# Performance work log

Hardware: AMD Instinct MI355X
Metric: run time of the kernel (lower is better)

Reference implementation:

```python
import jax, jax.numpy as jnp
import numpy as np

V = 50000
E = 300000
B = 4
LAT = 512
H = 128
L = 3


def setup_inputs() -> dict:
    key = jax.random.key(0)
    ks = jax.random.split(key, 8)
    vertex_xyz = jax.random.normal(ks[0], (V, 3), jnp.float32)
    latent = jax.random.normal(ks[1], (B, LAT), jnp.float32)
    edge_index = jax.random.randint(ks[2], (2, E), 0, V, dtype=jnp.int32)
    def lin(k, out_f, in_f):
        return jax.random.normal(k, (out_f, in_f), jnp.float32) / np.float32(np.sqrt(in_f))
    W_in = lin(ks[3], H, LAT + 3)
    b_in = jnp.zeros((H,), jnp.float32)
    conv_W = jax.random.normal(ks[4], (L, H, H), jnp.float32) / np.float32(np.sqrt(H))
    conv_b = jnp.zeros((L, H), jnp.float32)
    W_out = lin(ks[5], 3, H)
    b_out = jnp.zeros((3,), jnp.float32)
    return dict(vertex_xyz=vertex_xyz, latent=latent, edge_index=edge_index,
                W_in=W_in, b_in=b_in, conv_W=conv_W, conv_b=conv_b,
                W_out=W_out, b_out=b_out)


def _edge_norm(edge_index, B_, V_):
    """GCN symmetric normalization for edge_index tiled B times (same node ids,
    as in the original code's edge_index.repeat(1, B)) plus self-loops on all
    N = B*V flattened nodes. Structure is identical across layers, so compute once."""
    N = B_ * V_
    ei = jnp.tile(edge_index, (1, B_))                 # (2, E*B), ids in [0, V)
    loops = jnp.arange(N, dtype=edge_index.dtype)
    row = jnp.concatenate([ei[0], loops])              # source
    col = jnp.concatenate([ei[1], loops])              # target
    deg = jax.ops.segment_sum(jnp.ones(row.shape, jnp.float32), col, num_segments=N)
    dis = jnp.where(deg > 0, jax.lax.rsqrt(jnp.maximum(deg, 1.0)), 0.0)
    norm = dis[row] * dis[col]                         # (E*B + N,)
    return row, col, norm, N


def reference(vertex_xyz, latent, edge_index, W_in, b_in, conv_W, conv_b, W_out, b_out):
    B_, V_ = latent.shape[0], vertex_xyz.shape[0]
    row, col, norm, N = _edge_norm(edge_index, B_, V_)

    # concat template xyz with broadcast latent -> (B*V, LAT+3)
    x = jnp.concatenate([
        jnp.broadcast_to(vertex_xyz[None], (B_, V_, 3)),
        jnp.broadcast_to(latent[:, None, :], (B_, V_, latent.shape[-1])),
    ], axis=-1).reshape(B_ * V_, -1)

    x = jax.nn.relu(x @ W_in.T + b_in)                 # (N, H)

    for l in range(conv_W.shape[0]):
        h = x @ conv_W[l].T                            # linear (no bias before aggregation)
        agg = jax.ops.segment_sum(norm[:, None] * h[row], col, num_segments=N)
        x = jax.nn.relu(agg + conv_b[l])

    out = x @ W_out.T + b_out                          # (N, 3)
    return out.reshape(B_, V_, 3)
```

## Files before the change

### kernel.cpp

```cpp
#include <hip/hip_runtime.h>
#include <hip/hip_bf16.h>

typedef __attribute__((ext_vector_type(8))) short short8;
typedef __attribute__((ext_vector_type(4))) float f32x4;

#define V_ 50000
#define E_ 300000
#define B_ 4
#define LAT_ 512
#define H_ 128
#define L_ 3
#define N_ (B_*V_)

#define SCAN_B 512
#define SCAN_G ((V_ + SCAN_B - 1) / SCAN_B)


__global__ void k_zero(int* __restrict__ deg, int* __restrict__ cursor) {
    int i = blockIdx.x * 256 + threadIdx.x;
    if (i < V_) { deg[i] = 0; cursor[i] = 0; }
}

__global__ void k_deg(const int* __restrict__ dst, int* __restrict__ deg) {
    int e = blockIdx.x * 256 + threadIdx.x;
    if (e < E_) atomicAdd(&deg[dst[e]], 1);
}

__global__ __launch_bounds__(SCAN_B) void k_scan1(const int* __restrict__ deg,
                                                  int* __restrict__ off,
                                                  float* __restrict__ dis,
                                                  int* __restrict__ part) {
    int t = threadIdx.x;
    int i = blockIdx.x * SCAN_B + t;
    int d = (i < V_) ? deg[i] : 0;
    __shared__ int sm[SCAN_B];
    sm[t] = d;
    __syncthreads();
    int val = d;
    for (int s = 1; s < SCAN_B; s <<= 1) {
        int o = (t >= s) ? sm[t - s] : 0;
        __syncthreads();
        val += o;
        sm[t] = val;
        __syncthreads();
    }
    if (i < V_) {
        off[i] = val - d;
        dis[i] = rsqrtf((float)(B_ * d + 1));
    }
    if (t == SCAN_B - 1) part[blockIdx.x] = val;
}

__global__ void k_scan2(int* __restrict__ part) {
    __shared__ int sm[128];
    int t = threadIdx.x;
    int v = (t < SCAN_G) ? part[t] : 0;
    sm[t] = v;
    __syncthreads();
    int val = v;
    for (int s = 1; s < 128; s <<= 1) {
        int o = (t >= s) ? sm[t - s] : 0;
        __syncthreads();
        val += o;
        sm[t] = val;
        __syncthreads();
    }
    if (t < SCAN_G) part[t] = val - v;
}

__global__ __launch_bounds__(SCAN_B) void k_scan3(int* __restrict__ off,
                                                  const int* __restrict__ part) {
    int i = blockIdx.x * SCAN_B + threadIdx.x;
    if (i < V_) off[i] += part[blockIdx.x];
    if (i == 0) off[V_] = E_;
}

__global__ void k_fill(const int* __restrict__ src, const int* __restrict__ dst,
                       const int* __restrict__ off, int* __restrict__ cursor,
                       int* __restrict__ csr) {
    int e = blockIdx.x * 256 + threadIdx.x;
    if (e < E_) {
        int c = dst[e];
        int p = atomicAdd(&cursor[c], 1);
        csr[off[c] + p] = src[e];
    }
}


__global__ void k_wsplit(const float* __restrict__ W, ushort* __restrict__ Whi,
                         ushort* __restrict__ Wlo) {
    int i = blockIdx.x * 256 + threadIdx.x;
    float w = W[i];
    __hip_bfloat16 hb = __float2bfloat16(w);
    float hf = __bfloat162float(hb);
    __hip_bfloat16 lb = __float2bfloat16(w - hf);
    Whi[i] = *(ushort*)&hb;
    Wlo[i] = *(ushort*)&lb;
}


__global__ void k_latproj(const float* __restrict__ Win, const float* __restrict__ bin,
                          const float* __restrict__ latent, float* __restrict__ latproj) {
    int t = blockIdx.x * 128 + threadIdx.x;
    if (t >= B_ * H_) return;
    int b = t >> 7, j = t & 127;
    const float* wr = Win + (size_t)j * (LAT_ + 3) + 3;
    const float* lp = latent + (size_t)b * LAT_;
    float s = bin[j];
    for (int k = 0; k < LAT_; k++) s = fmaf(wr[k], lp[k], s);
    latproj[t] = s;
}

__global__ void k_x0(const float* __restrict__ xyz, const float* __restrict__ Win,
                     const float* __restrict__ latproj,
                     ushort* __restrict__ xh, ushort* __restrict__ xl) {
    size_t idx = (size_t)blockIdx.x * 256 + threadIdx.x;
    int j = (int)(idx & 127);
    size_t node = idx >> 7;
    int v = (int)(node % V_);
    int b = (int)(node / V_);
    const float* wr = Win + (size_t)j * (LAT_ + 3);
    float s = latproj[b * H_ + j];
    s = fmaf(wr[0], xyz[v * 3 + 0], s);
    s = fmaf(wr[1], xyz[v * 3 + 1], s);
    s = fmaf(wr[2], xyz[v * 3 + 2], s);
    s = fmaxf(s, 0.f);
    __hip_bfloat16 hb = __float2bfloat16(s);
    float hf = __bfloat162float(hb);
    __hip_bfloat16 lb = __float2bfloat16(s - hf);
    xh[idx] = *(ushort*)&hb;
    xl[idx] = *(ushort*)&lb;
}


#define LDSB 33792

__global__ __launch_bounds__(512) void k_layer(const ushort* __restrict__ xh,
                                               const ushort* __restrict__ xl,
                                               const ushort* __restrict__ Wh,
                                               const ushort* __restrict__ Wl,
                                               const float* __restrict__ bias,
                                               float* __restrict__ h,
                                               ushort* __restrict__ xh_out,
                                               ushort* __restrict__ xl_out) {
    __shared__ __align__(16) char smem[LDSB];
    const int tid = threadIdx.x;
    const int row0 = blockIdx.x * 64;
    const int lane = tid & 63;
    const int wid  = tid >> 6;
    const int l15  = lane & 15;
    const int kg   = lane >> 4;
    const int n0   = wid * 16;

    short8 wf[2][4];
    {
        const ushort* Wp[2] = {Wh, Wl};
#pragma unroll
        for (int p = 0; p < 2; p++)
#pragma unroll
            for (int ks = 0; ks < 4; ks++) {
                const ushort* b = Wp[p] + (size_t)(n0 + l15) * 128 + ks * 32 + kg * 4;
                union { short8 v; uint2 u[2]; } u;
                u.u[0] = *(const uint2*)(b);
                u.u[1] = *(const uint2*)(b + 16);
                wf[p][ks] = u.v;
            }
    }

    {
        const ushort* xp[2] = {xh, xl};
#pragma unroll
        for (int p = 0; p < 2; p++) {
            char* base = smem + p * 16384;
#pragma unroll
            for (int rep = 0; rep < 2; rep++) {
                int chunk = tid + rep * 512;
                int r  = chunk >> 4;
                int cb = (chunk & 15) * 16;
                uint4 g = *(const uint4*)((const char*)(xp[p] + (size_t)(row0 + r) * 128) + cb);
                *(uint4*)(base + r * 256 + (cb ^ ((r & 7) << 4))) = g;
            }
        }
    }
    __syncthreads();

    f32x4 acc[4];
#pragma unroll
    for (int mt = 0; mt < 4; mt++) acc[mt] = (f32x4){0.f, 0.f, 0.f, 0.f};
#pragma unroll
    for (int mt = 0; mt < 4; mt++) {
        int row = mt * 16 + l15;
        const char* rbh = smem + row * 256;
        const char* rbl = smem + 16384 + row * 256;
        const int swz = (row & 7) << 4;
#pragma unroll
        for (int ks = 0; ks < 4; ks++) {
            int c0 = ks * 64 + kg * 8;
            union { short8 v; uint2 u[2]; } ah, al;
            ah.u[0] = *(const uint2*)(rbh + ((c0) ^ swz));
            ah.u[1] = *(const uint2*)(rbh + ((c0 + 32) ^ swz));
            al.u[0] = *(const uint2*)(rbl + ((c0) ^ swz));
            al.u[1] = *(const uint2*)(rbl + ((c0 + 32) ^ swz));
            acc[mt] = __builtin_amdgcn_mfma_f32_16x16x32_bf16(ah.v, wf[0][ks], acc[mt], 0, 0, 0);
            acc[mt] = __builtin_amdgcn_mfma_f32_16x16x32_bf16(al.v, wf[0][ks], acc[mt], 0, 0, 0);
            acc[mt] = __builtin_amdgcn_mfma_f32_16x16x32_bf16(ah.v, wf[1][ks], acc[mt], 0, 0, 0);
        }
    }
    __syncthreads();

    float* bb = (float*)smem;
#pragma unroll
    for (int mt = 0; mt < 4; mt++)
#pragma unroll
        for (int j = 0; j < 4; j++)
            bb[(mt * 16 + kg * 4 + j) * 132 + n0 + l15] = acc[mt][j];
    __syncthreads();

    {
        int r  = tid >> 3;
        int c0 = (tid & 7) * 16;
        int grow = row0 + r;
        float v[16];
#pragma unroll
        for (int i = 0; i < 16; i += 4) {
            f32x4 q = *(const f32x4*)(&bb[r * 132 + c0 + i]);
            v[i + 0] = q[0]; v[i + 1] = q[1]; v[i + 2] = q[2]; v[i + 3] = q[3];
        }
        if (grow < V_) {
            float* hp = h + (size_t)grow * 128 + c0;
#pragma unroll
            for (int i = 0; i < 16; i += 4) {
                f32x4 q = {v[i], v[i + 1], v[i + 2], v[i + 3]};
                *(f32x4*)(hp + i) = q;
            }
        } else {
            ushort hs[16], ls[16];
#pragma unroll
            for (int i = 0; i < 16; i++) {
                float vv = fmaxf(v[i] + bias[c0 + i], 0.f);
                __hip_bfloat16 hb = __float2bfloat16(vv);
                float hf = __bfloat162float(hb);
                __hip_bfloat16 lb = __float2bfloat16(vv - hf);
                hs[i] = *(ushort*)&hb;
                ls[i] = *(ushort*)&lb;
            }
            char* ph = (char*)(xh_out + (size_t)grow * 128 + c0);
            char* pl = (char*)(xl_out + (size_t)grow * 128 + c0);
            *(uint4*)(ph)      = *(uint4*)&hs[0];
            *(uint4*)(ph + 16) = *(uint4*)&hs[8];
            *(uint4*)(pl)      = *(uint4*)&ls[0];
            *(uint4*)(pl + 16) = *(uint4*)&ls[8];
        }
    }
}


__global__ __launch_bounds__(256) void k_agg0(const float* __restrict__ h,
                                              const float* __restrict__ dis,
                                              const int* __restrict__ off,
                                              const int* __restrict__ csr,
                                              const float* __restrict__ bias,
                                              ushort* __restrict__ xh_out,
                                              ushort* __restrict__ xl_out) {
    int c = blockIdx.x * 4 + (threadIdx.x >> 6);
    int lane = threadIdx.x & 63;
    if (c >= V_) return;
    float dc = dis[c];
    float a0 = 0.f, a1 = 0.f;
    int beg = off[c], end = off[c + 1];
    for (int i = beg; i < end; i++) {
        int u = csr[i];
        float wu = dis[u];
        const float* hu = h + (size_t)u * 128;
        a0 = fmaf(wu, hu[lane],      a0);
        a1 = fmaf(wu, hu[lane + 64], a1);
    }
    const float* hr = h + (size_t)c * 128;
    float s0 = fmaxf(dc * (float)B_ * a0 + dc * dc * hr[lane]      + bias[lane],      0.f);
    float s1 = fmaxf(dc * (float)B_ * a1 + dc * dc * hr[lane + 64] + bias[lane + 64], 0.f);
    __hip_bfloat16 h0 = __float2bfloat16(s0);
    __hip_bfloat16 l0 = __float2bfloat16(s0 - __bfloat162float(h0));
    __hip_bfloat16 h1 = __float2bfloat16(s1);
    __hip_bfloat16 l1 = __float2bfloat16(s1 - __bfloat162float(h1));
    xh_out[(size_t)c * 128 + lane]      = *(ushort*)&h0;
    xl_out[(size_t)c * 128 + lane]      = *(ushort*)&l0;
    xh_out[(size_t)c * 128 + lane + 64] = *(ushort*)&h1;
    xl_out[(size_t)c * 128 + lane + 64] = *(ushort*)&l1;
}


__global__ __launch_bounds__(256) void k_out(const ushort* __restrict__ xh,
                                             const ushort* __restrict__ xl,
                                             const float* __restrict__ Wout,
                                             const float* __restrict__ bout,
                                             float* __restrict__ out) {
    int n = (int)(((size_t)blockIdx.x * 256 + threadIdx.x) >> 6);
    int lane = threadIdx.x & 63;
    if (n >= N_) return;
    const ushort* ph = xh + (size_t)n * 128;
    const ushort* pl = xl + (size_t)n * 128;
    ushort u0h = ph[lane], u0l = pl[lane], u1h = ph[lane + 64], u1l = pl[lane + 64];
    float x0 = __bfloat162float(*(__hip_bfloat16*)&u0h) + __bfloat162float(*(__hip_bfloat16*)&u0l);
    float x1 = __bfloat162float(*(__hip_bfloat16*)&u1h) + __bfloat162float(*(__hip_bfloat16*)&u1l);
#pragma unroll
    for (int o = 0; o < 3; o++) {
        float a = x0 * Wout[o * 128 + lane] + x1 * Wout[o * 128 + 64 + lane];
#pragma unroll
        for (int d = 32; d; d >>= 1) a += __shfl_down(a, d);
        if (lane == 0) out[(size_t)n * 3 + o] = a + bout[o];
    }
}


extern "C" void kernel_launch(void* const* d_in, const int* in_sizes, int n_in,
                              void* d_out, int out_size, void* d_ws, size_t ws_size,
                              hipStream_t stream) {
    const float* xyz    = (const float*)d_in[0];
    const float* latent = (const float*)d_in[1];
    const int*   ei     = (const int*)d_in[2];
    const float* Win    = (const float*)d_in[3];
    const float* bin    = (const float*)d_in[4];
    const float* convW  = (const float*)d_in[5];
    const float* convb  = (const float*)d_in[6];
    const float* Wout   = (const float*)d_in[7];
    const float* bout   = (const float*)d_in[8];
    float* out = (float*)d_out;

    char* w = (char*)d_ws;
    auto carve = [&](size_t bytes) {
        char* p = w;
        w += (bytes + 255) & ~(size_t)255;
        return p;
    };
    ushort* xh      = (ushort*)carve((size_t)N_ * H_ * 2);
    ushort* xl      = (ushort*)carve((size_t)N_ * H_ * 2);
    float*  h       = (float*)carve((size_t)V_ * H_ * 4);
    ushort* Whi     = (ushort*)carve((size_t)L_ * H_ * H_ * 2);
    ushort* Wlo     = (ushort*)carve((size_t)L_ * H_ * H_ * 2);
    float*  dis     = (float*)carve((size_t)V_ * 4);
    float*  latproj = (float*)carve((size_t)B_ * H_ * 4);
    int*    deg     = (int*)carve((size_t)V_ * 4);
    int*    off     = (int*)carve((size_t)(V_ + 1) * 4);
    int*    cursor  = (int*)carve((size_t)V_ * 4);
    int*    csr     = (int*)carve((size_t)E_ * 4);
    int*    part    = (int*)carve((size_t)SCAN_G * 4);
    (void)ws_size; (void)in_sizes; (void)n_in; (void)out_size;

    const int* src = ei;
    const int* dst = ei + E_;

    k_zero<<<(V_ + 255) / 256, 256, 0, stream>>>(deg, cursor);
    k_deg<<<(E_ + 255) / 256, 256, 0, stream>>>(dst, deg);
    k_scan1<<<SCAN_G, SCAN_B, 0, stream>>>(deg, off, dis, part);
    k_scan2<<<1, 128, 0, stream>>>(part);
    k_scan3<<<SCAN_G, SCAN_B, 0, stream>>>(off, part);
    k_fill<<<(E_ + 255) / 256, 256, 0, stream>>>(src, dst, off, cursor, csr);

    k_wsplit<<<(L_ * H_ * H_) / 256, 256, 0, stream>>>(convW, Whi, Wlo);
    k_latproj<<<4, 128, 0, stream>>>(Win, bin, latent, latproj);
    k_x0<<<(int)(((size_t)N_ * H_) / 256), 256, 0, stream>>>(xyz, Win, latproj, xh, xl);

    for (int l = 0; l < L_; l++) {
        k_layer<<<N_ / 64, 512, 0, stream>>>(xh, xl,
                                             Whi + (size_t)l * H_ * H_,
                                             Wlo + (size_t)l * H_ * H_,
                                             convb + (size_t)l * H_,
                                             h, xh, xl);
        k_agg0<<<(V_ + 3) / 4, 256, 0, stream>>>(h, dis, off, csr,
                                                 convb + (size_t)l * H_, xh, xl);
    }

    k_out<<<N_ / 4, 256, 0, stream>>>(xh, xl, Wout, bout, out);
}
```

Measured before the change: 504.4 us.

## Fuse all layers for edge-free batches into one LDS-resident kernel

Nodes in batches 1..B-1 have only self-loops, so each layer reduces to a pointwise linear+relu. A single kernel now runs input projection, all three layers and the output head for those rows while keeping activations in LDS, which removes the global round trips of x/h for three quarters of the nodes. Batch 0 keeps the separate GEMM and CSR-aggregation kernels, with the input projection fused into the first GEMM and the output head fused into the last aggregation. Neighbor indices are also preloaded per wave and broadcast with shuffles. The cost is a 64KB-LDS kernel with lower occupancy, plus more specialized code paths.

```diff
diff --git a/kernel.cpp b/kernel.cpp
--- a/kernel.cpp
+++ b/kernel.cpp
@@ -14,6 +14,18 @@
 
 #define SCAN_B 512
 #define SCAN_G ((V_ + SCAN_B - 1) / SCAN_B)
+
+__device__ inline void bsplit(float v, ushort& hi, ushort& lo) {
+    __hip_bfloat16 hb = __float2bfloat16(v);
+    float hf = __bfloat162float(hb);
+    __hip_bfloat16 lb = __float2bfloat16(v - hf);
+    hi = *(ushort*)&hb; lo = *(ushort*)&lb;
+}
+__device__ inline float bjoin(ushort h, ushort l) {
+    __hip_bfloat16 hb = *(__hip_bfloat16*)&h;
+    __hip_bfloat16 lb = *(__hip_bfloat16*)&l;
+    return __bfloat162float(hb) + __bfloat162float(lb);
+}
 
 
 __global__ void k_zero(int* __restrict__ deg, int* __restrict__ cursor) {
@@ -91,13 +103,9 @@
                          ushort* __restrict__ Wlo) {
     int i = blockIdx.x * 256 + threadIdx.x;
     float w = W[i];
-    __hip_bfloat16 hb = __float2bfloat16(w);
-    float hf = __bfloat162float(hb);
-    __hip_bfloat16 lb = __float2bfloat16(w - hf);
-    Whi[i] = *(ushort*)&hb;
-    Wlo[i] = *(ushort*)&lb;
-}
-
+    ushort hi, lo; bsplit(w, hi, lo);
+    Whi[i] = hi; Wlo[i] = lo;
+}
 
 __global__ void k_latproj(const float* __restrict__ Win, const float* __restrict__ bin,
                           const float* __restrict__ latent, float* __restrict__ latproj) {
@@ -111,203 +119,336 @@
     latproj[t] = s;
 }
 
-__global__ void k_x0(const float* __restrict__ xyz, const float* __restrict__ Win,
-                     const float* __restrict__ latproj,
-                     ushort* __restrict__ xh, ushort* __restrict__ xl) {
-    size_t idx = (size_t)blockIdx.x * 256 + threadIdx.x;
-    int j = (int)(idx & 127);
-    size_t node = idx >> 7;
-    int v = (int)(node % V_);
-    int b = (int)(node / V_);
-    const float* wr = Win + (size_t)j * (LAT_ + 3);
-    float s = latproj[b * H_ + j];
-    s = fmaf(wr[0], xyz[v * 3 + 0], s);
-    s = fmaf(wr[1], xyz[v * 3 + 1], s);
-    s = fmaf(wr[2], xyz[v * 3 + 2], s);
-    s = fmaxf(s, 0.f);
-    __hip_bfloat16 hb = __float2bfloat16(s);
-    float hf = __bfloat162float(hb);
-    __hip_bfloat16 lb = __float2bfloat16(s - hf);
-    xh[idx] = *(ushort*)&hb;
-    xl[idx] = *(ushort*)&lb;
-}
-
-
-#define LDSB 33792
-
-__global__ __launch_bounds__(512) void k_layer(const ushort* __restrict__ xh,
-                                               const ushort* __restrict__ xl,
-                                               const ushort* __restrict__ Wh,
-                                               const ushort* __restrict__ Wl,
-                                               const float* __restrict__ bias,
-                                               float* __restrict__ h,
-                                               ushort* __restrict__ xh_out,
-                                               ushort* __restrict__ xl_out) {
-    __shared__ __align__(16) char smem[LDSB];
+
+__global__ __launch_bounds__(512, 4) void k_big(
+        const float* __restrict__ xyz, const float* __restrict__ latproj,
+        const float* __restrict__ Win,
+        const ushort* __restrict__ Whi, const ushort* __restrict__ Wlo,
+        const float* __restrict__ convb,
+        const float* __restrict__ Wout, const float* __restrict__ bout,
+        float* __restrict__ out) {
+    __shared__ __align__(16) char smem[65536];
     const int tid = threadIdx.x;
-    const int row0 = blockIdx.x * 64;
+    const int row0 = V_ + blockIdx.x * 64;
     const int lane = tid & 63;
     const int wid  = tid >> 6;
     const int l15  = lane & 15;
     const int kg   = lane >> 4;
     const int n0   = wid * 16;
-
-    short8 wf[2][4];
-    {
-        const ushort* Wp[2] = {Wh, Wl};
-#pragma unroll
-        for (int p = 0; p < 2; p++)
-#pragma unroll
-            for (int ks = 0; ks < 4; ks++) {
-                const ushort* b = Wp[p] + (size_t)(n0 + l15) * 128 + ks * 32 + kg * 4;
-                union { short8 v; uint2 u[2]; } u;
-                u.u[0] = *(const uint2*)(b);
-                u.u[1] = *(const uint2*)(b + 16);
-                wf[p][ks] = u.v;
-            }
-    }
-
-    {
-        const ushort* xp[2] = {xh, xl};
-#pragma unroll
-        for (int p = 0; p < 2; p++) {
-            char* base = smem + p * 16384;
-#pragma unroll
-            for (int rep = 0; rep < 2; rep++) {
-                int chunk = tid + rep * 512;
-                int r  = chunk >> 4;
-                int cb = (chunk & 15) * 16;
-                uint4 g = *(const uint4*)((const char*)(xp[p] + (size_t)(row0 + r) * 128) + cb);
-                *(uint4*)(base + r * 256 + (cb ^ ((r & 7) << 4))) = g;
-            }
-        }
-    }
-    __syncthreads();
-
-    f32x4 acc[4];
-#pragma unroll
-    for (int mt = 0; mt < 4; mt++) acc[mt] = (f32x4){0.f, 0.f, 0.f, 0.f};
-#pragma unroll
-    for (int mt = 0; mt < 4; mt++) {
-        int row = mt * 16 + l15;
-        const char* rbh = smem + row * 256;
-        const char* rbl = smem + 16384 + row * 256;
-        const int swz = (row & 7) << 4;
-#pragma unroll
-        for (int ks = 0; ks < 4; ks++) {
-            int c0 = ks * 64 + kg * 8;
-            union { short8 v; uint2 u[2]; } ah, al;
-            ah.u[0] = *(const uint2*)(rbh + ((c0) ^ swz));
-            ah.u[1] = *(const uint2*)(rbh + ((c0 + 32) ^ swz));
-            al.u[0] = *(const uint2*)(rbl + ((c0) ^ swz));
-            al.u[1] = *(const uint2*)(rbl + ((c0 + 32) ^ swz));
-            acc[mt] = __builtin_amdgcn_mfma_f32_16x16x32_bf16(ah.v, wf[0][ks], acc[mt], 0, 0, 0);
-            acc[mt] = __builtin_amdgcn_mfma_f32_16x16x32_bf16(al.v, wf[0][ks], acc[mt], 0, 0, 0);
-            acc[mt] = __builtin_amdgcn_mfma_f32_16x16x32_bf16(ah.v, wf[1][ks], acc[mt], 0, 0, 0);
-        }
-    }
-    __syncthreads();
-
-    float* bb = (float*)smem;
-#pragma unroll
-    for (int mt = 0; mt < 4; mt++)
-#pragma unroll
-        for (int j = 0; j < 4; j++)
-            bb[(mt * 16 + kg * 4 + j) * 132 + n0 + l15] = acc[mt][j];
-    __syncthreads();
-
-    {
-        int r  = tid >> 3;
-        int c0 = (tid & 7) * 16;
-        int grow = row0 + r;
-        float v[16];
-#pragma unroll
-        for (int i = 0; i < 16; i += 4) {
-            f32x4 q = *(const f32x4*)(&bb[r * 132 + c0 + i]);
-            v[i + 0] = q[0]; v[i + 1] = q[1]; v[i + 2] = q[2]; v[i + 3] = q[3];
-        }
-        if (grow < V_) {
-            float* hp = h + (size_t)grow * 128 + c0;
-#pragma unroll
-            for (int i = 0; i < 16; i += 4) {
-                f32x4 q = {v[i], v[i + 1], v[i + 2], v[i + 3]};
-                *(f32x4*)(hp + i) = q;
+    const int tr   = tid >> 4;
+    const int c0   = (tid & 15) * 8;
+
+#pragma unroll
+    for (int rep = 0; rep < 2; rep++) {
+        int row = tr + rep * 32;
+        int node = row0 + row;
+        ushort hs[8], ls[8];
+        if (node < N_) {
+            int v = node % V_, b = node / V_;
+            float xv0 = xyz[v*3+0], xv1 = xyz[v*3+1], xv2 = xyz[v*3+2];
+#pragma unroll
+            for (int i = 0; i < 8; i++) {
+                int j = c0 + i;
+                float s = latproj[b*H_ + j];
+                s = fmaf(Win[(size_t)j*(LAT_+3)+0], xv0, s);
+                s = fmaf(Win[(size_t)j*(LAT_+3)+1], xv1, s);
+                s = fmaf(Win[(size_t)j*(LAT_+3)+2], xv2, s);
+                s = fmaxf(s, 0.f);
+                bsplit(s, hs[i], ls[i]);
             }
         } else {
-            ushort hs[16], ls[16];
-#pragma unroll
-            for (int i = 0; i < 16; i++) {
-                float vv = fmaxf(v[i] + bias[c0 + i], 0.f);
-                __hip_bfloat16 hb = __float2bfloat16(vv);
-                float hf = __bfloat162float(hb);
-                __hip_bfloat16 lb = __float2bfloat16(vv - hf);
-                hs[i] = *(ushort*)&hb;
-                ls[i] = *(ushort*)&lb;
+#pragma unroll
+            for (int i = 0; i < 8; i++) { hs[i] = 0; ls[i] = 0; }
+        }
+        int bo = (c0*2) ^ ((row & 7) << 4);
+        *(uint4*)(smem + row*256 + bo) = *(uint4*)hs;
+        *(uint4*)(smem + 16384 + row*256 + bo) = *(uint4*)ls;
+    }
+    __syncthreads();
+
+    int cur = 0;
+    for (int l = 0; l < L_; l++) {
+        const ushort* Whp = Whi + (size_t)l*H_*H_;
+        const ushort* Wlp = Wlo + (size_t)l*H_*H_;
+        short8 wh[4], wl[4];
+#pragma unroll
+        for (int ks = 0; ks < 4; ks++) {
+            const ushort* bh = Whp + (size_t)(n0 + l15)*H_ + ks*32 + kg*4;
+            const ushort* bl = Wlp + (size_t)(n0 + l15)*H_ + ks*32 + kg*4;
+            union { short8 v; uint2 u[2]; } uh, ul;
+            uh.u[0] = *(const uint2*)bh;  uh.u[1] = *(const uint2*)(bh + 16);
+            ul.u[0] = *(const uint2*)bl;  ul.u[1] = *(const uint2*)(bl + 16);
+            wh[ks] = uh.v; wl[ks] = ul.v;
+        }
+        const char* sb = smem + cur*32768;
+        f32x4 acc[4];
+#pragma unroll
+        for (int mt = 0; mt < 4; mt++) acc[mt] = (f32x4){0.f,0.f,0.f,0.f};
+#pragma unroll
+        for (int mt = 0; mt < 4; mt++) {
+            int row = mt*16 + l15;
+            int swz = (row & 7) << 4;
+            const char* rbh = sb + row*256;
+            const char* rbl = sb + 16384 + row*256;
+#pragma unroll
+            for (int ks = 0; ks < 4; ks++) {
+                int cc = ks*64 + kg*8;
+                union { short8 v; uint2 u[2]; } ah, al;
+                ah.u[0] = *(const uint2*)(rbh + (cc ^ swz));
+                ah.u[1] = *(const uint2*)(rbh + ((cc+32) ^ swz));
+                al.u[0] = *(const uint2*)(rbl + (cc ^ swz));
+                al.u[1] = *(const uint2*)(rbl + ((cc+32) ^ swz));
+                acc[mt] = __builtin_amdgcn_mfma_f32_16x16x32_bf16(ah.v, wh[ks], acc[mt], 0,0,0);
+                acc[mt] = __builtin_amdgcn_mfma_f32_16x16x32_bf16(al.v, wh[ks], acc[mt], 0,0,0);
+                acc[mt] = __builtin_amdgcn_mfma_f32_16x16x32_bf16(ah.v, wl[ks], acc[mt], 0,0,0);
             }
-            char* ph = (char*)(xh_out + (size_t)grow * 128 + c0);
-            char* pl = (char*)(xl_out + (size_t)grow * 128 + c0);
-            *(uint4*)(ph)      = *(uint4*)&hs[0];
-            *(uint4*)(ph + 16) = *(uint4*)&hs[8];
-            *(uint4*)(pl)      = *(uint4*)&ls[0];
-            *(uint4*)(pl + 16) = *(uint4*)&ls[8];
-        }
-    }
-}
-
-
+        }
+        __syncthreads();
+        char* db = smem + (cur^1)*32768;
+        float bv = convb[l*H_ + n0 + l15];
+        int bo = (n0 + l15) * 2;
+#pragma unroll
+        for (int mt = 0; mt < 4; mt++)
+#pragma unroll
+            for (int j = 0; j < 4; j++) {
+                int row = mt*16 + kg*4 + j;
+                int swz = (row & 7) << 4;
+                float v = fmaxf(acc[mt][j] + bv, 0.f);
+                ushort hi, lo; bsplit(v, hi, lo);
+                *(ushort*)(db + row*256 + (bo ^ swz)) = hi;
+                *(ushort*)(db + 16384 + row*256 + (bo ^ swz)) = lo;
+            }
+        __syncthreads();
+        cur ^= 1;
+    }
+
+    const char* ob = smem + cur*32768;
+    float wo0[8], wo1[8], wo2[8];
+#pragma unroll
+    for (int i = 0; i < 8; i++) {
+        wo0[i] = Wout[0*H_ + c0 + i];
+        wo1[i] = Wout[1*H_ + c0 + i];
+        wo2[i] = Wout[2*H_ + c0 + i];
+    }
+#pragma unroll
+    for (int rep = 0; rep < 2; rep++) {
+        int row = tr + rep*32;
+        int node = row0 + row;
+        int bo = (c0*2) ^ ((row & 7) << 4);
+        uint4 uh = *(const uint4*)(ob + row*256 + bo);
+        uint4 ul = *(const uint4*)(ob + 16384 + row*256 + bo);
+        const ushort* hp = (const ushort*)&uh;
+        const ushort* lp = (const ushort*)&ul;
+        float p0 = 0.f, p1 = 0.f, p2 = 0.f;
+#pragma unroll
+        for (int i = 0; i < 8; i++) {
+            float xv = bjoin(hp[i], lp[i]);
+            p0 = fmaf(xv, wo0[i], p0);
+            p1 = fmaf(xv, wo1[i], p1);
+            p2 = fmaf(xv, wo2[i], p2);
+        }
+#pragma unroll
+        for (int m = 1; m < 16; m <<= 1) {
+            p0 += __shfl_xor(p0, m);
+            p1 += __shfl_xor(p1, m);
+            p2 += __shfl_xor(p2, m);
+        }
+        if ((tid & 15) == 0 && node < N_) {
+            out[(size_t)node*3 + 0] = p0 + bout[0];
+            out[(size_t)node*3 + 1] = p1 + bout[1];
+            out[(size_t)node*3 + 2] = p2 + bout[2];
+        }
+    }
+}
+
+
+template<int MODE>
+__global__ __launch_bounds__(256, 4) void k_layerb0(
+        const ushort* __restrict__ xh, const ushort* __restrict__ xl,
+        const float* __restrict__ xyz, const float* __restrict__ latproj,
+        const float* __restrict__ Win,
+        const ushort* __restrict__ Whp, const ushort* __restrict__ Wlp,
+        float* __restrict__ h) {
+    __shared__ __align__(16) char smem[16896];
+    const int tid = threadIdx.x;
+    const int row0 = blockIdx.x * 32;
+    const int lane = tid & 63;
+    const int wid  = tid >> 6;
+    const int l15  = lane & 15;
+    const int kg   = lane >> 4;
+    const int n0   = wid * 32;
+    const int tr   = tid >> 4;
+    const int c0   = (tid & 15) * 8;
+
+    if (MODE == 0) {
+#pragma unroll
+        for (int rep = 0; rep < 2; rep++) {
+            int row = tr + rep * 16;
+            int v = row0 + row;
+            ushort hs[8], ls[8];
+            if (v < V_) {
+                float xv0 = xyz[v*3+0], xv1 = xyz[v*3+1], xv2 = xyz[v*3+2];
+#pragma unroll
+                for (int i = 0; i < 8; i++) {
+                    int j = c0 + i;
+                    float s = latproj[j];
+                    s = fmaf(Win[(size_t)j*(LAT_+3)+0], xv0, s);
+                    s = fmaf(Win[(size_t)j*(LAT_+3)+1], xv1, s);
+                    s = fmaf(Win[(size_t)j*(LAT_+3)+2], xv2, s);
+                    s = fmaxf(s, 0.f);
+                    bsplit(s, hs[i], ls[i]);
+                }
+            } else {
+#pragma unroll
+                for (int i = 0; i < 8; i++) { hs[i] = 0; ls[i] = 0; }
+            }
+            int bo = (c0*2) ^ ((row & 7) << 4);
+            *(uint4*)(smem + row*256 + bo) = *(uint4*)hs;
+            *(uint4*)(smem + 8192 + row*256 + bo) = *(uint4*)ls;
+        }
+    } else {
+#pragma unroll
+        for (int k = 0; k < 4; k++) {
+            int chunk = tid + k*256;
+            int p  = chunk >> 9;
+            int r  = (chunk >> 4) & 31;
+            int cb = (chunk & 15) * 16;
+            int grow = row0 + r;
+            uint4 g = {0u,0u,0u,0u};
+            if (grow < V_)
+                g = *(const uint4*)((const char*)((p ? xl : xh) + (size_t)grow*H_) + cb);
+            *(uint4*)(smem + p*8192 + r*256 + (cb ^ ((r & 7) << 4))) = g;
+        }
+    }
+    __syncthreads();
+
+    short8 wh[2][4], wl[2][4];
+#pragma unroll
+    for (int nt = 0; nt < 2; nt++)
+#pragma unroll
+        for (int ks = 0; ks < 4; ks++) {
+            const ushort* bh = Whp + (size_t)(n0 + nt*16 + l15)*H_ + ks*32 + kg*4;
+            const ushort* bl = Wlp + (size_t)(n0 + nt*16 + l15)*H_ + ks*32 + kg*4;
+            union { short8 v; uint2 u[2]; } uh, ul;
+            uh.u[0] = *(const uint2*)bh;  uh.u[1] = *(const uint2*)(bh + 16);
+            ul.u[0] = *(const uint2*)bl;  ul.u[1] = *(const uint2*)(bl + 16);
+            wh[nt][ks] = uh.v; wl[nt][ks] = ul.v;
+        }
+
+    f32x4 acc[2][2];
+#pragma unroll
+    for (int mt = 0; mt < 2; mt++)
+#pragma unroll
+        for (int nt = 0; nt < 2; nt++) acc[mt][nt] = (f32x4){0.f,0.f,0.f,0.f};
+#pragma unroll
+    for (int mt = 0; mt < 2; mt++) {
+        int row = mt*16 + l15;
+        int swz = (row & 7) << 4;
+        const char* rbh = smem + row*256;
+        const char* rbl = smem + 8192 + row*256;
+#pragma unroll
+        for (int ks = 0; ks < 4; ks++) {
+            int cc = ks*64 + kg*8;
+            union { short8 v; uint2 u[2]; } ah, al;
+            ah.u[0] = *(const uint2*)(rbh + (cc ^ swz));
+            ah.u[1] = *(const uint2*)(rbh + ((cc+32) ^ swz));
+            al.u[0] = *(const uint2*)(rbl + (cc ^ swz));
+            al.u[1] = *(const uint2*)(rbl + ((cc+32) ^ swz));
+#pragma unroll
+            for (int nt = 0; nt < 2; nt++) {
+                acc[mt][nt] = __builtin_amdgcn_mfma_f32_16x16x32_bf16(ah.v, wh[nt][ks], acc[mt][nt], 0,0,0);
+                acc[mt][nt] = __builtin_amdgcn_mfma_f32_16x16x32_bf16(al.v, wh[nt][ks], acc[mt][nt], 0,0,0);
+                acc[mt][nt] = __builtin_amdgcn_mfma_f32_16x16x32_bf16(ah.v, wl[nt][ks], acc[mt][nt], 0,0,0);
+            }
+        }
+    }
+    __syncthreads();
+
+    float* bb = (float*)smem;
+#pragma unroll
+    for (int mt = 0; mt < 2; mt++)
+#pragma unroll
+        for (int nt = 0; nt < 2; nt++)
+#pragma unroll
+            for (int j = 0; j < 4; j++)
+                bb[(mt*16 + kg*4 + j)*132 + n0 + nt*16 + l15] = acc[mt][nt][j];
+    __syncthreads();
+
+#pragma unroll
+    for (int rep = 0; rep < 2; rep++) {
+        int row = tr + rep*16;
+        int grow = row0 + row;
+        if (grow < V_) {
+            f32x4 a = *(const f32x4*)&bb[row*132 + c0];
+            f32x4 b = *(const f32x4*)&bb[row*132 + c0 + 4];
+            *(f32x4*)(h + (size_t)grow*H_ + c0)     = a;
+            *(f32x4*)(h + (size_t)grow*H_ + c0 + 4) = b;
+        }
+    }
+}
+
+
+template<bool FINAL>
 __global__ __launch_bounds__(256) void k_agg0(const float* __restrict__ h,
                                               const float* __restrict__ dis,
                                               const int* __restrict__ off,
                                               const int* __restrict__ csr,
                                               const float* __restrict__ bias,
                                               ushort* __restrict__ xh_out,
-                                              ushort* __restrict__ xl_out) {
+                                              ushort* __restrict__ xl_out,
+                                              const float* __restrict__ Wout,
+                                              const float* __restrict__ bout,
+                                              float* __restrict__ out) {
     int c = blockIdx.x * 4 + (threadIdx.x >> 6);
     int lane = threadIdx.x & 63;
     if (c >= V_) return;
-    float dc = dis[c];
+    int beg = off[c], end = off[c + 1];
+    int nu = end - beg;
+    int   myu  = (lane < nu) ? csr[beg + lane] : 0;
+    float mywu = (lane < nu) ? dis[myu] : 0.f;
     float a0 = 0.f, a1 = 0.f;
-    int beg = off[c], end = off[c + 1];
-    for (int i = beg; i < end; i++) {
+    int nn = nu < 64 ? nu : 64;
+    for (int i = 0; i < nn; i++) {
+        int u = __shfl(myu, i);
+        float wu = __shfl(mywu, i);
+        const float* hu = h + (size_t)u * 128;
+        a0 = fmaf(wu, hu[lane],      a0);
+        a1 = fmaf(wu, hu[lane + 64], a1);
+    }
+    for (int i = beg + 64; i < end; i++) {
         int u = csr[i];
         float wu = dis[u];
         const float* hu = h + (size_t)u * 128;
         a0 = fmaf(wu, hu[lane],      a0);
         a1 = fmaf(wu, hu[lane + 64], a1);
     }
+    float dc = dis[c];
     const float* hr = h + (size_t)c * 128;
     float s0 = fmaxf(dc * (float)B_ * a0 + dc * dc * hr[lane]      + bias[lane],      0.f);
     float s1 = fmaxf(dc * (float)B_ * a1 + dc * dc * hr[lane + 64] + bias[lane + 64], 0.f);
-    __hip_bfloat16 h0 = __float2bfloat16(s0);
-    __hip_bfloat16 l0 = __float2bfloat16(s0 - __bfloat162float(h0));
-    __hip_bfloat16 h1 = __float2bfloat16(s1);
-    __hip_bfloat16 l1 = __float2bfloat16(s1 - __bfloat162float(h1));
-    xh_out[(size_t)c * 128 + lane]      = *(ushort*)&h0;
-    xl_out[(size_t)c * 128 + lane]      = *(ushort*)&l0;
-    xh_out[(size_t)c * 128 + lane + 64] = *(ushort*)&h1;
-    xl_out[(size_t)c * 128 + lane + 64] = *(ushort*)&l1;
-}
-
-
-__global__ __launch_bounds__(256) void k_out(const ushort* __restrict__ xh,
-                                             const ushort* __restrict__ xl,
-                                             const float* __restrict__ Wout,
-                                             const float* __restrict__ bout,
-                                             float* __restrict__ out) {
-    int n = (int)(((size_t)blockIdx.x * 256 + threadIdx.x) >> 6);
-    int lane = threadIdx.x & 63;
-    if (n >= N_) return;
-    const ushort* ph = xh + (size_t)n * 128;
-    const ushort* pl = xl + (size_t)n * 128;
-    ushort u0h = ph[lane], u0l = pl[lane], u1h = ph[lane + 64], u1l = pl[lane + 64];
-    float x0 = __bfloat162float(*(__hip_bfloat16*)&u0h) + __bfloat162float(*(__hip_bfloat16*)&u0l);
-    float x1 = __bfloat162float(*(__hip_bfloat16*)&u1h) + __bfloat162float(*(__hip_bfloat16*)&u1l);
-#pragma unroll
-    for (int o = 0; o < 3; o++) {
-        float a = x0 * Wout[o * 128 + lane] + x1 * Wout[o * 128 + 64 + lane];
-#pragma unroll
-        for (int d = 32; d; d >>= 1) a += __shfl_down(a, d);
-        if (lane == 0) out[(size_t)n * 3 + o] = a + bout[o];
+    if (FINAL) {
+        float p0 = s0 * Wout[0*H_ + lane] + s1 * Wout[0*H_ + 64 + lane];
+        float p1 = s0 * Wout[1*H_ + lane] + s1 * Wout[1*H_ + 64 + lane];
+        float p2 = s0 * Wout[2*H_ + lane] + s1 * Wout[2*H_ + 64 + lane];
+#pragma unroll
+        for (int d = 32; d; d >>= 1) {
+            p0 += __shfl_down(p0, d);
+            p1 += __shfl_down(p1, d);
+            p2 += __shfl_down(p2, d);
+        }
+        if (lane == 0) {
+            out[(size_t)c*3 + 0] = p0 + bout[0];
+            out[(size_t)c*3 + 1] = p1 + bout[1];
+            out[(size_t)c*3 + 2] = p2 + bout[2];
+        }
+    } else {
+        ushort h0, l0, h1, l1;
+        bsplit(s0, h0, l0);
+        bsplit(s1, h1, l1);
+        xh_out[(size_t)c*128 + lane]      = h0;
+        xl_out[(size_t)c*128 + lane]      = l0;
+        xh_out[(size_t)c*128 + lane + 64] = h1;
+        xl_out[(size_t)c*128 + lane + 64] = l1;
     }
 }
 
@@ -332,8 +473,8 @@
         w += (bytes + 255) & ~(size_t)255;
         return p;
     };
-    ushort* xh      = (ushort*)carve((size_t)N_ * H_ * 2);
-    ushort* xl      = (ushort*)carve((size_t)N_ * H_ * 2);
+    ushort* xh      = (ushort*)carve((size_t)V_ * H_ * 2);
+    ushort* xl      = (ushort*)carve((size_t)V_ * H_ * 2);
     float*  h       = (float*)carve((size_t)V_ * H_ * 4);
     ushort* Whi     = (ushort*)carve((size_t)L_ * H_ * H_ * 2);
     ushort* Wlo     = (ushort*)carve((size_t)L_ * H_ * H_ * 2);
@@ -358,17 +499,21 @@
 
     k_wsplit<<<(L_ * H_ * H_) / 256, 256, 0, stream>>>(convW, Whi, Wlo);
     k_latproj<<<4, 128, 0, stream>>>(Win, bin, latent, latproj);
-    k_x0<<<(int)(((size_t)N_ * H_) / 256), 256, 0, stream>>>(xyz, Win, latproj, xh, xl);
-
-    for (int l = 0; l < L_; l++) {
-        k_layer<<<N_ / 64, 512, 0, stream>>>(xh, xl,
-                                             Whi + (size_t)l * H_ * H_,
-                                             Wlo + (size_t)l * H_ * H_,
-                                             convb + (size_t)l * H_,
-                                             h, xh, xl);
-        k_agg0<<<(V_ + 3) / 4, 256, 0, stream>>>(h, dis, off, csr,
-                                                 convb + (size_t)l * H_, xh, xl);
-    }
-
-    k_out<<<N_ / 4, 256, 0, stream>>>(xh, xl, Wout, bout, out);
-}
+
+    k_big<<<(N_ - V_ + 63) / 64, 512, 0, stream>>>(xyz, latproj, Win, Whi, Wlo,
+                                                   convb, Wout, bout, out);
+
+    const int GB0 = (V_ + 31) / 32;
+    k_layerb0<0><<<GB0, 256, 0, stream>>>(nullptr, nullptr, xyz, latproj, Win,
+                                          Whi, Wlo, h);
+    k_agg0<false><<<(V_ + 3) / 4, 256, 0, stream>>>(h, dis, off, csr, convb,
+                                                    xh, xl, nullptr, nullptr, nullptr);
+    k_layerb0<1><<<GB0, 256, 0, stream>>>(xh, xl, nullptr, nullptr, nullptr,
+                                          Whi + (size_t)1*H_*H_, Wlo + (size_t)1*H_*H_, h);
+    k_agg0<false><<<(V_ + 3) / 4, 256, 0, stream>>>(h, dis, off, csr, convb + 1*H_,
+                                                    xh, xl, nullptr, nullptr, nullptr);
+    k_layerb0<1><<<GB0, 256, 0, stream>>>(xh, xl, nullptr, nullptr, nullptr,
+                                          Whi + (size_t)2*H_*H_, Wlo + (size_t)2*H_*H_, h);
+    k_agg0<true><<<(V_ + 3) / 4, 256, 0, stream>>>(h, dis, off, csr, convb + 2*H_,
+                                                   nullptr, nullptr, Wout, bout, out);
+}
```

Result: faster. 436.3 us (-13.5%).
